# Kernel tuning notes

Measured on AMD Instinct MI355X. Metric: run time of the kernel, lower is better.

Reference implementation:

```python
import jax, jax.numpy as jnp
import numpy as np
from jax import lax

PAD = (3, 3)
PAD_VALUE = -1.0
POOL_SIZE = 7
POOL_STRIDE = 2


def setup_inputs() -> dict:
    key = jax.random.key(0)
    k1, k2 = jax.random.split(key)
    B, Cin, L = 64, 64, 16384
    Cout, K = 128, 7
    I = jax.random.normal(k1, (B, Cin, L), dtype=jnp.float32)
    W = jax.random.normal(k2, (Cout, Cin, K), dtype=jnp.float32)
    # Threshold params are initialized to ones in the module (requires_grad=False)
    threshold_plus = jnp.ones((Cout,), dtype=jnp.float32)
    threshold_minus = jnp.ones((Cout,), dtype=jnp.float32)
    threshold_plus_sign = jnp.ones((Cout,), dtype=jnp.float32)
    threshold_minus_sign = jnp.ones((Cout,), dtype=jnp.float32)
    return {
        "I": I,
        "W": W,
        "threshold_plus": threshold_plus,
        "threshold_minus": threshold_minus,
        "threshold_plus_sign": threshold_plus_sign,
        "threshold_minus_sign": threshold_minus_sign,
    }


def reference(I, W, threshold_plus, threshold_minus, threshold_plus_sign, threshold_minus_sign):
    # 1) ConstantPad1d(padding=(3,3), value=-1.0)
    x = jnp.pad(I, ((0, 0), (0, 0), PAD), constant_values=PAD_VALUE)
    # 2) Binarize activations and weights via sign(), then float conv1d (no bias)
    ba = jnp.sign(x)
    bw = jnp.sign(W)
    conv = lax.conv_general_dilated(
        ba, bw,
        window_strides=(1,),
        padding="VALID",
        dimension_numbers=("NCH", "OIH", "NCH"),
    )  # [B, Cout, L]
    # 3) MaxPool1d(kernel_size=7, stride=2)
    pooled = lax.reduce_window(
        conv, -jnp.inf, lax.max,
        window_dimensions=(1, 1, POOL_SIZE),
        window_strides=(1, 1, POOL_STRIDE),
        padding="VALID",
    )  # [B, Cout, Lp]
    # 4) Per-channel Threshold (vectorized over channels; 2*c > 2*t == c > t)
    tp = threshold_plus[None, :, None]
    tm = threshold_minus[None, :, None]
    ps = threshold_plus_sign[None, :, None]
    ms = threshold_minus_sign[None, :, None]
    pos_branch = jnp.where(pooled > tp, ps, -ps)
    neg_branch = jnp.where(pooled > tm, ms, -ms)
    out = jnp.where(pooled >= 0, pos_branch, neg_branch)
    return out
```

## Files before the change

kernel.cpp:

```cpp
#include <hip/hip_runtime.h>
#include <stdint.h>

#define B_    64
#define CIN   64
#define L_IN  16384
#define COUT  128
#define K_    7
#define LPAD  3
#define LP    (L_IN + 2*LPAD)
#define LPA   16416
#define LOUT  8189
#define NTERMS 448
#define TOUT  8
#define CO_PER_BLK 16

__global__ __launch_bounds__(256) void pack_A(const float* __restrict__ I,
                                              uint64_t* __restrict__ A) {
    int b     = blockIdx.x >> 4;
    int chunk = blockIdx.x & 15;
    int t     = threadIdx.x;
    int l0    = chunk * 1024 + t * 4;
    const uint32_t* Ib = (const uint32_t*)(I + (size_t)b * CIN * L_IN + l0);
    uint32_t lo0 = 0, lo1 = 0, lo2 = 0, lo3 = 0;
    uint32_t hi0 = 0, hi1 = 0, hi2 = 0, hi3 = 0;
#pragma unroll 8
    for (int ci = 0; ci < 32; ++ci) {
        uint4 v = *(const uint4*)(Ib + (size_t)ci * L_IN);
        lo0 |= (v.x >> 31) << ci;
        lo1 |= (v.y >> 31) << ci;
        lo2 |= (v.z >> 31) << ci;
        lo3 |= (v.w >> 31) << ci;
    }
#pragma unroll 8
    for (int ci = 0; ci < 32; ++ci) {
        uint4 v = *(const uint4*)(Ib + (size_t)(ci + 32) * L_IN);
        hi0 |= (v.x >> 31) << ci;
        hi1 |= (v.y >> 31) << ci;
        hi2 |= (v.z >> 31) << ci;
        hi3 |= (v.w >> 31) << ci;
    }
    uint64_t* Ab = A + (size_t)b * LPA + (LPAD + l0);
    Ab[0] = ((uint64_t)hi0 << 32) | lo0;
    Ab[1] = ((uint64_t)hi1 << 32) | lo1;
    Ab[2] = ((uint64_t)hi2 << 32) | lo2;
    Ab[3] = ((uint64_t)hi3 << 32) | lo3;
    if (chunk == 0 && t < 6) {
        int l = (t < 3) ? t : (L_IN + t);
        A[(size_t)b * LPA + l] = ~0ULL;
    }
}

__global__ __launch_bounds__(256) void pack_W(const float* __restrict__ W,
                                              uint64_t* __restrict__ Bp) {
    int idx = blockIdx.x * 256 + threadIdx.x;
    if (idx >= COUT * K_) return;
    int co = idx / K_, k = idx - co * K_;
    uint64_t acc = 0;
#pragma unroll
    for (int ci = 0; ci < CIN; ++ci) {
        uint32_t s = __float_as_uint(W[(size_t)co * CIN * K_ + ci * K_ + k]) >> 31;
        acc |= (uint64_t)s << ci;
    }
    Bp[idx] = acc;
}

__global__ __launch_bounds__(256, 4) void bconv_pool_thresh(
    const uint64_t* __restrict__ A, const uint64_t* __restrict__ Bp,
    const float* __restrict__ tp_, const float* __restrict__ tm_,
    const float* __restrict__ ps_, const float* __restrict__ ms_,
    float* __restrict__ out)
{
    const int cg = blockIdx.x;
    const int lc = blockIdx.y;
    const int b  = blockIdx.z;
    const int t  = threadIdx.x;
    int out0 = lc * 2048 + t * TOUT;
    if (out0 > LOUT - TOUT) out0 = LOUT - TOUT;

    const uint64_t* Ab = A + (size_t)b * LPA + 2 * out0;
    uint64_t a[2 * TOUT + 11];
#pragma unroll
    for (int j = 0; j < 2 * TOUT + 11; ++j) a[j] = Ab[j];

#pragma unroll 1
    for (int ci_ = 0; ci_ < CO_PER_BLK; ++ci_) {
        const int co = cg * CO_PER_BLK + ci_;
        const uint64_t* Bco = Bp + co * K_;
        const uint64_t w0 = Bco[0], w1 = Bco[1], w2 = Bco[2], w3 = Bco[3],
                       w4 = Bco[4], w5 = Bco[5], w6 = Bco[6];

        int s[2 * TOUT + 5];
#pragma unroll
        for (int j = 0; j < 2 * TOUT + 5; ++j) {
            int acc;
            acc  = __popcll(a[j + 0] ^ w0);
            acc += __popcll(a[j + 1] ^ w1);
            acc += __popcll(a[j + 2] ^ w2);
            acc += __popcll(a[j + 3] ^ w3);
            acc += __popcll(a[j + 4] ^ w4);
            acc += __popcll(a[j + 5] ^ w5);
            acc += __popcll(a[j + 6] ^ w6);
            s[j] = acc;
        }

        int p[TOUT + 2];
#pragma unroll
        for (int i = 0; i < TOUT + 2; ++i) p[i] = min(s[2 * i], s[2 * i + 1]);

        const float ftp = (448.0f - tp_[co]) * 0.5f;
        const float ftm = (448.0f - tm_[co]) * 0.5f;
        const float ps = ps_[co], ms = ms_[co];
        float* op = out + ((size_t)(b * COUT + co)) * LOUT + out0;
#pragma unroll
        for (int o = 0; o < TOUT; ++o) {
            int smin = min(min(p[o], p[o + 1]), min(p[o + 2], s[2 * o + 6]));
            float sf  = (float)smin;
            float pos = sf < ftp ? ps : -ps;
            float neg = sf < ftm ? ms : -ms;
            op[o] = (sf <= 224.0f) ? pos : neg;
        }
    }
}

extern "C" void kernel_launch(void* const* d_in, const int* in_sizes, int n_in,
                              void* d_out, int out_size, void* d_ws, size_t ws_size,
                              hipStream_t stream) {
    const float* I  = (const float*)d_in[0];
    const float* W  = (const float*)d_in[1];
    const float* tp = (const float*)d_in[2];
    const float* tm = (const float*)d_in[3];
    const float* ps = (const float*)d_in[4];
    const float* ms = (const float*)d_in[5];
    float* out = (float*)d_out;

    uint64_t* A  = (uint64_t*)d_ws;
    uint64_t* Bp = (uint64_t*)((char*)d_ws + (size_t)B_ * LPA * sizeof(uint64_t));

    hipLaunchKernelGGL(pack_A, dim3(B_ * 16), dim3(256), 0, stream, I, A);
    hipLaunchKernelGGL(pack_W, dim3((COUT * K_ + 255) / 256), dim3(256), 0, stream, W, Bp);
    hipLaunchKernelGGL(bconv_pool_thresh, dim3(8, 4, B_), dim3(256), 0, stream,
                       A, Bp, tp, tm, ps, ms, out);
}
```

Before: 597.7 us.

## Replace XOR-popcount binary conv with int8 MFMA conv via LDS tiles

```diff
diff --git a/kernel.cpp b/kernel.cpp
--- a/kernel.cpp
+++ b/kernel.cpp
@@ -7,12 +7,14 @@
 #define COUT  128
 #define K_    7
 #define LPAD  3
-#define LP    (L_IN + 2*LPAD)
 #define LPA   16416
 #define LOUT  8189
-#define NTERMS 448
-#define TOUT  8
-#define CO_PER_BLK 16
+#define OB    120
+#define NXB   69
+#define XROWS 264
+#define CSTR  260
+
+typedef int v4i __attribute__((ext_vector_type(4)));
 
 __global__ __launch_bounds__(256) void pack_A(const float* __restrict__ I,
                                               uint64_t* __restrict__ A) {
@@ -50,74 +52,133 @@
     }
 }
 
-__global__ __launch_bounds__(256) void pack_W(const float* __restrict__ W,
-                                              uint64_t* __restrict__ Bp) {
+__global__ __launch_bounds__(256) void pack_Wi8(const float* __restrict__ W,
+                                                uint8_t* __restrict__ Wp) {
     int idx = blockIdx.x * 256 + threadIdx.x;
     if (idx >= COUT * K_) return;
-    int co = idx / K_, k = idx - co * K_;
-    uint64_t acc = 0;
-#pragma unroll
-    for (int ci = 0; ci < CIN; ++ci) {
-        uint32_t s = __float_as_uint(W[(size_t)co * CIN * K_ + ci * K_ + k]) >> 31;
-        acc |= (uint64_t)s << ci;
-    }
-    Bp[idx] = acc;
-}
-
-__global__ __launch_bounds__(256, 4) void bconv_pool_thresh(
-    const uint64_t* __restrict__ A, const uint64_t* __restrict__ Bp,
+    int k  = idx >> 7;
+    int co = idx & 127;
+    uint8_t* dst = Wp + ((size_t)k * COUT + co) * 64;
+    uint32_t d[16];
+#pragma unroll
+    for (int ci4 = 0; ci4 < 16; ++ci4) {
+        uint32_t dw = 0;
+#pragma unroll
+        for (int j = 0; j < 4; ++j) {
+            int ci = ci4 * 4 + j;
+            uint32_t s = __float_as_uint(W[(size_t)co * CIN * K_ + ci * K_ + k]) >> 31;
+            dw |= (s ? 0xFFu : 0x01u) << (8 * j);
+        }
+        d[ci4] = dw;
+    }
+#pragma unroll
+    for (int q = 0; q < 4; ++q)
+        *(uint4*)(dst + q * 16) = make_uint4(d[4*q+0], d[4*q+1], d[4*q+2], d[4*q+3]);
+}
+
+__global__ __launch_bounds__(256) void mfma_conv_pool(
+    const uint64_t* __restrict__ A, const uint8_t* __restrict__ Wp,
     const float* __restrict__ tp_, const float* __restrict__ tm_,
     const float* __restrict__ ps_, const float* __restrict__ ms_,
     float* __restrict__ out)
 {
-    const int cg = blockIdx.x;
-    const int lc = blockIdx.y;
-    const int b  = blockIdx.z;
-    const int t  = threadIdx.x;
-    int out0 = lc * 2048 + t * TOUT;
-    if (out0 > LOUT - TOUT) out0 = LOUT - TOUT;
-
-    const uint64_t* Ab = A + (size_t)b * LPA + 2 * out0;
-    uint64_t a[2 * TOUT + 11];
-#pragma unroll
-    for (int j = 0; j < 2 * TOUT + 11; ++j) a[j] = Ab[j];
+    __shared__ __align__(16) uint8_t xs[XROWS * 64];
+    __shared__ __align__(8)  int16_t cs[64 * CSTR];
+
+    const int bx = blockIdx.x, cy = blockIdx.y, b = blockIdx.z;
+    const int t = threadIdx.x;
+    const int lane = t & 63, w = t >> 6;
+    const int l15 = lane & 15, l4 = lane >> 4;
+    const int o0 = bx * OB;
+    const int c0 = 2 * o0;
+    const int cout0 = cy * 64;
+
+    const uint16_t* ap = (const uint16_t*)(A + (size_t)b * LPA);
+#pragma unroll
+    for (int it = 0; it < 5; ++it) {
+        int idx = it * 256 + t;
+        if (idx < XROWS * 4) {
+            int p = idx >> 2, g = idx & 3;
+            int pg = c0 + p;
+            if (pg < LPA) {
+                uint32_t v = ap[(size_t)pg * 4 + g];
+                uint32_t dd[4];
+#pragma unroll
+                for (int ni = 0; ni < 4; ++ni) {
+                    uint32_t n  = (v >> (4 * ni)) & 0xFu;
+                    uint32_t tb = (n & 1u) | ((n & 2u) << 7) | ((n & 4u) << 14) | ((n & 8u) << 21);
+                    dd[ni] = 0x01010101u ^ (tb * 0xFEu);
+                }
+                int gran = g ^ ((p >> 1) & 3);
+                *(uint4*)(xs + p * 64 + gran * 16) = make_uint4(dd[0], dd[1], dd[2], dd[3]);
+            }
+        }
+    }
+
+    v4i wf[4][7];
+#pragma unroll
+    for (int ct = 0; ct < 4; ++ct)
+#pragma unroll
+        for (int k = 0; k < K_; ++k)
+            wf[ct][k] = *(const v4i*)(Wp + (((size_t)k * COUT + cout0 + ct * 16 + l15) * 64 + l4 * 16));
+
+    __syncthreads();
+
+#pragma unroll
+    for (int j = 0; j < 4; ++j) {
+        const int ctile = w * 4 + j;
+        v4i af[K_];
+#pragma unroll
+        for (int k = 0; k < K_; ++k) {
+            int pl   = ctile * 16 + l15 + k;
+            int gran = l4 ^ ((pl >> 1) & 3);
+            af[k] = *(const v4i*)(xs + pl * 64 + gran * 16);
+        }
+        v4i ac0 = {0,0,0,0}, ac1 = {0,0,0,0}, ac2 = {0,0,0,0}, ac3 = {0,0,0,0};
+#pragma unroll
+        for (int k = 0; k < K_; ++k) {
+            ac0 = __builtin_amdgcn_mfma_i32_16x16x64_i8(af[k], wf[0][k], ac0, 0, 0, 0);
+            ac1 = __builtin_amdgcn_mfma_i32_16x16x64_i8(af[k], wf[1][k], ac1, 0, 0, 0);
+            ac2 = __builtin_amdgcn_mfma_i32_16x16x64_i8(af[k], wf[2][k], ac2, 0, 0, 0);
+            ac3 = __builtin_amdgcn_mfma_i32_16x16x64_i8(af[k], wf[3][k], ac3, 0, 0, 0);
+        }
+        const int crow = ctile * 16 + l4 * 4;
+        {
+            uint32_t p0, p1;
+            int16_t* dst;
+#define STORE_CT(ac, CT) \
+            p0 = ((uint32_t)(ac)[0] & 0xFFFFu) | ((uint32_t)(ac)[1] << 16); \
+            p1 = ((uint32_t)(ac)[2] & 0xFFFFu) | ((uint32_t)(ac)[3] << 16); \
+            dst = cs + (size_t)((CT) * 16 + l15) * CSTR + crow; \
+            *(uint2*)dst = make_uint2(p0, p1);
+            STORE_CT(ac0, 0) STORE_CT(ac1, 1) STORE_CT(ac2, 2) STORE_CT(ac3, 3)
+#undef STORE_CT
+        }
+    }
+    __syncthreads();
 
 #pragma unroll 1
-    for (int ci_ = 0; ci_ < CO_PER_BLK; ++ci_) {
-        const int co = cg * CO_PER_BLK + ci_;
-        const uint64_t* Bco = Bp + co * K_;
-        const uint64_t w0 = Bco[0], w1 = Bco[1], w2 = Bco[2], w3 = Bco[3],
-                       w4 = Bco[4], w5 = Bco[5], w6 = Bco[6];
-
-        int s[2 * TOUT + 5];
-#pragma unroll
-        for (int j = 0; j < 2 * TOUT + 5; ++j) {
-            int acc;
-            acc  = __popcll(a[j + 0] ^ w0);
-            acc += __popcll(a[j + 1] ^ w1);
-            acc += __popcll(a[j + 2] ^ w2);
-            acc += __popcll(a[j + 3] ^ w3);
-            acc += __popcll(a[j + 4] ^ w4);
-            acc += __popcll(a[j + 5] ^ w5);
-            acc += __popcll(a[j + 6] ^ w6);
-            s[j] = acc;
-        }
-
-        int p[TOUT + 2];
-#pragma unroll
-        for (int i = 0; i < TOUT + 2; ++i) p[i] = min(s[2 * i], s[2 * i + 1]);
-
-        const float ftp = (448.0f - tp_[co]) * 0.5f;
-        const float ftm = (448.0f - tm_[co]) * 0.5f;
+    for (int ci = 0; ci < 16; ++ci) {
+        const int cl = w * 16 + ci;
+        const int co = cout0 + cl;
+        const int Tip = (int)floorf(tp_[co]) + 1;
+        const int Tim = (int)floorf(tm_[co]) + 1;
         const float ps = ps_[co], ms = ms_[co];
-        float* op = out + ((size_t)(b * COUT + co)) * LOUT + out0;
-#pragma unroll
-        for (int o = 0; o < TOUT; ++o) {
-            int smin = min(min(p[o], p[o + 1]), min(p[o + 2], s[2 * o + 6]));
-            float sf  = (float)smin;
-            float pos = sf < ftp ? ps : -ps;
-            float neg = sf < ftm ? ms : -ms;
-            op[o] = (sf <= 224.0f) ? pos : neg;
+        const uint32_t* row = (const uint32_t*)(cs + (size_t)cl * CSTR);
+        float* op = out + ((size_t)(b * COUT + co)) * LOUT + o0;
+#pragma unroll
+        for (int oi = 0; oi < 2; ++oi) {
+            int o = oi * 64 + lane;
+            if (o < OB && o0 + o < LOUT) {
+                uint32_t d0 = row[o], d1 = row[o+1], d2 = row[o+2], d3 = row[o+3];
+                int a0 = (int)(short)(d0 & 0xFFFFu), a1 = ((int)d0) >> 16;
+                int a2 = (int)(short)(d1 & 0xFFFFu), a3 = ((int)d1) >> 16;
+                int a4 = (int)(short)(d2 & 0xFFFFu), a5 = ((int)d2) >> 16;
+                int a6 = (int)(short)(d3 & 0xFFFFu);
+                int m = max(max(max(a0, a1), max(a2, a3)), max(max(a4, a5), a6));
+                float r = (m >= 0) ? (m >= Tip ? ps : -ps) : (m >= Tim ? ms : -ms);
+                op[o] = r;
+            }
         }
     }
 }
@@ -134,10 +195,10 @@
     float* out = (float*)d_out;
 
     uint64_t* A  = (uint64_t*)d_ws;
-    uint64_t* Bp = (uint64_t*)((char*)d_ws + (size_t)B_ * LPA * sizeof(uint64_t));
+    uint8_t*  Wp = (uint8_t*)((char*)d_ws + (size_t)B_ * LPA * sizeof(uint64_t));
 
     hipLaunchKernelGGL(pack_A, dim3(B_ * 16), dim3(256), 0, stream, I, A);
-    hipLaunchKernelGGL(pack_W, dim3((COUT * K_ + 255) / 256), dim3(256), 0, stream, W, Bp);
-    hipLaunchKernelGGL(bconv_pool_thresh, dim3(8, 4, B_), dim3(256), 0, stream,
-                       A, Bp, tp, tm, ps, ms, out);
-}
+    hipLaunchKernelGGL(pack_Wi8, dim3((COUT * K_ + 255) / 256), dim3(256), 0, stream, W, Wp);
+    hipLaunchKernelGGL(mfma_conv_pool, dim3(NXB, 2, B_), dim3(256), 0, stream,
+                       A, Wp, tp, tm, ps, ms, out);
+}
```

Result: slower. 644.5 us (+7.8%).
